# Kernel optimization log

Hardware: AMD Instinct MI355X
Metric: run time of the kernel (lower is better)

The kernel has to match this reference:

```python
import jax, jax.numpy as jnp
import numpy as np

N_NODES = 50000
N_EDGES = 800000
FEA_DIM = 128
N_LAYER = 3
ACTOR_H = 512
N_GRAPHS = 64


def gcn_conv(x, src, dst, W, b, n_nodes):
    """PyG GCNConv: add self-loops, symmetric deg normalization, linear, scatter-add.
    out[i] = sum_{j->i} d_j^{-1/2} d_i^{-1/2} (x_j W) + d_i^{-1} (x_i W) + b
    where d_i = in_degree(i) + 1 (self-loop included)."""
    h = x @ W  # [N, F]
    deg = jax.ops.segment_sum(jnp.ones(src.shape[0], x.dtype), dst, num_segments=n_nodes) + 1.0
    dinv = jax.lax.rsqrt(deg)  # [N]
    coef = (dinv[src] * dinv[dst])[:, None]  # [E, 1]
    agg = jax.ops.segment_sum(h[src] * coef, dst, num_segments=n_nodes)  # gather-scale-scatter
    agg = agg + h * (dinv * dinv)[:, None]  # self-loop term
    return agg + b


def setup_inputs() -> dict:
    key = jax.random.key(0)
    ks = jax.random.split(key, 12)
    x = jax.random.normal(ks[0], (N_NODES, FEA_DIM), dtype=jnp.float32)
    edge_index = jax.random.randint(ks[1], (2, N_EDGES), 0, N_NODES, dtype=jnp.int32)
    batch = jnp.sort(jax.random.randint(ks[2], (N_NODES,), 0, N_GRAPHS, dtype=jnp.int32))
    s = 1.0 / np.sqrt(FEA_DIM)
    conv_W = jax.random.normal(ks[3], (N_LAYER, FEA_DIM, FEA_DIM), dtype=jnp.float32) * s
    conv_b = jnp.zeros((N_LAYER, FEA_DIM), dtype=jnp.float32)
    fea_w1 = jax.random.normal(ks[4], (FEA_DIM, ACTOR_H), dtype=jnp.float32) * s
    fea_b1 = jnp.zeros((ACTOR_H,), dtype=jnp.float32)
    fea_w2 = jax.random.normal(ks[5], (ACTOR_H, FEA_DIM), dtype=jnp.float32) * (1.0 / np.sqrt(ACTOR_H))
    fea_b2 = jnp.zeros((FEA_DIM,), dtype=jnp.float32)
    node_w = jax.random.normal(ks[6], (FEA_DIM, 1), dtype=jnp.float32) * s
    node_b = jnp.zeros((1,), dtype=jnp.float32)
    return {"x": x, "edge_index": edge_index, "batch": batch,
            "conv_W": conv_W, "conv_b": conv_b,
            "fea_w1": fea_w1, "fea_b1": fea_b1,
            "fea_w2": fea_w2, "fea_b2": fea_b2,
            "node_w": node_w, "node_b": node_b}


def reference(x, edge_index, batch, conv_W, conv_b, fea_w1, fea_b1, fea_w2, fea_b2, node_w, node_b):
    src, dst = edge_index[0], edge_index[1]
    n_nodes = x.shape[0]
    for l in range(N_LAYER):  # fixed small layer loop
        x = jax.nn.relu(gcn_conv(x, src, dst, conv_W[l], conv_b[l], n_nodes))
    node_prob = jnp.squeeze(x @ node_w + node_b, axis=-1)  # [N]
    # global mean pool over graphs
    sums = jax.ops.segment_sum(x, batch, num_segments=N_GRAPHS)  # [G, F]
    cnts = jax.ops.segment_sum(jnp.ones(n_nodes, x.dtype), batch, num_segments=N_GRAPHS)
    fea = sums / jnp.maximum(cnts, 1.0)[:, None]
    fea = jax.nn.relu(fea @ fea_w1 + fea_b1)
    fea_prob = fea @ fea_w2 + fea_b2  # [G, F]
    return (node_prob, fea_prob)
```

## Files before the change

### kernel.cpp

```cpp
#include <hip/hip_runtime.h>

#define N_NODES 50000
#define N_EDGES 800000
#define FEA 128
#define NL 3
#define AH 512
#define NG 64
#define NBLK 196

typedef short bf16x8 __attribute__((ext_vector_type(8)));
typedef float f32x4 __attribute__((ext_vector_type(4)));
typedef uint  u32x4 __attribute__((ext_vector_type(4)));

__device__ __forceinline__ ushort f2bf(float f) {
    uint u = __float_as_uint(f);
    uint r = u + 0x7FFFu + ((u >> 16) & 1u);
    return (ushort)(r >> 16);
}
__device__ __forceinline__ float bf2f(ushort u) {
    return __uint_as_float((uint)u << 16);
}

#define HS ((size_t)(N_NODES + 1) * 32)
#define XS ((size_t)N_NODES * 32)

#define DA 3125
#define DB (DA + 3125)
#define DC (DB + 192)
#define DD (DC + 1)
__global__ __launch_bounds__(256) void k_deg_prep(const int* __restrict__ dst,
                                                  int* __restrict__ deg,
                                                  ushort* __restrict__ rank,
                                                  const float* __restrict__ x,
                                                  ushort* __restrict__ X,
                                                  const float* __restrict__ convW,
                                                  ushort* __restrict__ WhiT,
                                                  ushort* __restrict__ WloT,
                                                  ushort* __restrict__ H) {
    int blk = blockIdx.x;
    if (blk < DA) {
        int i = blk * 256 + threadIdx.x;
        rank[i] = (ushort)atomicAdd(&deg[dst[i]], 1);
    } else if (blk < DB) {
        int i = (blk - DA) * 256 + threadIdx.x;
        int node = i >> 4, c8 = i & 15;
        const float* xr = x + (size_t)node * FEA + c8 * 8;
        float4 u0 = *(const float4*)xr;
        float4 u1 = *(const float4*)(xr + 4);
        float xs[8] = {u0.x, u0.y, u0.z, u0.w, u1.x, u1.y, u1.z, u1.w};
        ushort hs[8];
#pragma unroll
        for (int k = 0; k < 8; ++k) hs[k] = f2bf(xs[k]);
        u32x4 hv;
        hv.x = (uint)hs[0] | ((uint)hs[1] << 16);
        hv.y = (uint)hs[2] | ((uint)hs[3] << 16);
        hv.z = (uint)hs[4] | ((uint)hs[5] << 16);
        hv.w = (uint)hs[6] | ((uint)hs[7] << 16);
        *(u32x4*)(X + (size_t)(c8 >> 2) * XS + (size_t)node * 32 + (c8 & 3) * 8) = hv;
    } else if (blk < DC) {
        int t = (blk - DB) * 256 + threadIdx.x;
        int l = t >> 14, r = t & 16383;
        int k = r >> 7, c = r & 127;
        float w = convW[t];
        ushort h = f2bf(w);
        WhiT[(size_t)l * 16384 + c * FEA + k] = h;
        WloT[(size_t)l * 16384 + c * FEA + k] = f2bf(w - bf2f(h));
    } else {
        if (threadIdx.x < 64) {
            int c = threadIdx.x >> 4, j = threadIdx.x & 15;
            ((uint*)H)[(size_t)c * (HS / 2) + (size_t)N_NODES * 16 + j] = 0;
        }
    }
}

__device__ __forceinline__ int block_scan_incl(int v, int* wsum) {
    int lane = threadIdx.x & 63, w = threadIdx.x >> 6;
    int s = v;
#pragma unroll
    for (int off = 1; off < 64; off <<= 1) {
        int t = __shfl_up(s, off);
        if (lane >= off) s += t;
    }
    if (lane == 63) wsum[w] = s;
    __syncthreads();
    int woff = 0;
    for (int k = 0; k < w; ++k) woff += wsum[k];
    return woff + s;
}

__global__ __launch_bounds__(256) void k_scan1(const int* __restrict__ deg,
                                               int* __restrict__ rowptr,
                                               int* __restrict__ bsum,
                                               float* __restrict__ dinv) {
    __shared__ int wsum[4];
    int i = blockIdx.x * 256 + threadIdx.x;
    int v = (i < N_NODES) ? deg[i] : 0;
    int pv = (v + 7) & ~7;
    int incl = block_scan_incl(pv, wsum);
    if (i < N_NODES) {
        rowptr[i] = incl - pv;
        dinv[i] = rsqrtf((float)v + 1.0f);
    }
    if (threadIdx.x == 255) bsum[blockIdx.x] = incl;
}

__global__ __launch_bounds__(256) void k_scan2(int* __restrict__ bsum,
                                               int* __restrict__ boff,
                                               int* __restrict__ rowptr) {
    __shared__ int wsum[4];
    int v = (threadIdx.x < NBLK) ? bsum[threadIdx.x] : 0;
    int incl = block_scan_incl(v, wsum);
    if (threadIdx.x < NBLK) boff[threadIdx.x] = incl - v;
    if (threadIdx.x == NBLK - 1) rowptr[N_NODES] = incl;
}

__global__ __launch_bounds__(256) void k_scan3(int* __restrict__ rowptr,
                                               const int* __restrict__ boff) {
    int i = blockIdx.x * 256 + threadIdx.x;
    if (i < N_NODES) rowptr[i] += boff[blockIdx.x];
}

#define FA 3125
#define FB (FA + NBLK)
#define FC (FB + NBLK)
__global__ __launch_bounds__(256) void k_fill2(const int* __restrict__ src,
                                               const int* __restrict__ dst,
                                               const int* __restrict__ rowptr,
                                               const ushort* __restrict__ rank,
                                               const int* __restrict__ deg,
                                               const int* __restrict__ batch,
                                               ushort* __restrict__ eidx,
                                               int* __restrict__ gstart) {
    int blk = blockIdx.x;
    if (blk < FA) {
        int e = blk * 256 + threadIdx.x;
        eidx[rowptr[dst[e]] + (int)rank[e]] = (ushort)src[e];
    } else if (blk < FB) {
        int i = (blk - FA) * 256 + threadIdx.x;
        if (i < N_NODES) {
            int d = deg[i], r = rowptr[i];
            int pd = (d + 7) & ~7;
            for (int k = d; k < pd; ++k) eidx[r + k] = (ushort)N_NODES;
        }
    } else {
        int i = (blk - FB) * 256 + threadIdx.x;
        if (i < N_NODES) {
            int b = batch[i];
            int bp = (i == 0) ? -1 : batch[i - 1];
            for (int g = bp + 1; g <= b; ++g) gstart[g] = i;
            if (i == N_NODES - 1)
                for (int g = b + 1; g <= NG; ++g) gstart[g] = N_NODES;
        }
    }
}

__global__ __launch_bounds__(256) void k_gemm(const ushort* __restrict__ X,
                                              const ushort* __restrict__ WhiT,
                                              const ushort* __restrict__ WloT,
                                              const float* __restrict__ dinv,
                                              ushort* __restrict__ H) {
    const int wv = threadIdx.x >> 6;
    const int lane = threadIdx.x & 63;
    const int lr = lane & 15;
    const int lk = lane >> 4;

    bf16x8 bhi[2][4], blo[2][4];
#pragma unroll
    for (int ct = 0; ct < 2; ++ct) {
        int col = wv * 32 + ct * 16 + lr;
#pragma unroll
        for (int kf = 0; kf < 4; ++kf) {
            bhi[ct][kf] = *(const bf16x8*)(WhiT + (size_t)col * FEA + kf * 32 + lk * 8);
            blo[ct][kf] = *(const bf16x8*)(WloT + (size_t)col * FEA + kf * 32 + lk * 8);
        }
    }

    for (int rt = blockIdx.x; rt < N_NODES / 16; rt += gridDim.x) {
        int r0 = rt * 16;
        bf16x8 a[4];
#pragma unroll
        for (int kf = 0; kf < 4; ++kf) {
            a[kf] = *(const bf16x8*)(X + (size_t)kf * XS + (size_t)(r0 + lr) * 32 + lk * 8);
        }
        f32x4 acc0 = {0.f, 0.f, 0.f, 0.f};
        f32x4 acc1 = {0.f, 0.f, 0.f, 0.f};
#pragma unroll
        for (int kf = 0; kf < 4; ++kf) {
            acc0 = __builtin_amdgcn_mfma_f32_16x16x32_bf16(a[kf], bhi[0][kf], acc0, 0, 0, 0);
            acc0 = __builtin_amdgcn_mfma_f32_16x16x32_bf16(a[kf], blo[0][kf], acc0, 0, 0, 0);
            acc1 = __builtin_amdgcn_mfma_f32_16x16x32_bf16(a[kf], bhi[1][kf], acc1, 0, 0, 0);
            acc1 = __builtin_amdgcn_mfma_f32_16x16x32_bf16(a[kf], blo[1][kf], acc1, 0, 0, 0);
        }
#pragma unroll
        for (int reg = 0; reg < 4; ++reg) {
            int orow = r0 + lk * 4 + reg;
            float s = dinv[orow];
            H[(size_t)wv * HS + (size_t)orow * 32 + lr]      = f2bf(acc0[reg] * s);
            H[(size_t)wv * HS + (size_t)orow * 32 + 16 + lr] = f2bf(acc1[reg] * s);
        }
    }
}

#define GNPB 64
#define GNB ((N_NODES + GNPB - 1) / GNPB)
__global__ __launch_bounds__(256) void k_gather(const int* __restrict__ rowptr,
                                                const ushort* __restrict__ eidx,
                                                const float* __restrict__ dinv,
                                                const ushort* __restrict__ H,
                                                const float* __restrict__ b,
                                                ushort* __restrict__ X) {
    int c = blockIdx.x & 3;
    int node = (blockIdx.x >> 2) * GNPB + (threadIdx.x >> 2);
    int l4 = threadIdx.x & 3;
    if (node >= N_NODES) return;
    const uint4* Hs = (const uint4*)H + (size_t)c * (N_NODES + 1) * 4;
    int r0 = rowptr[node], r1 = rowptr[node + 1];

    float a[8] = {0.f, 0.f, 0.f, 0.f, 0.f, 0.f, 0.f, 0.f};
#define ACC8(u)                                                              \
    do {                                                                     \
        a[0] += __uint_as_float((u).x << 16);                                \
        a[1] += __uint_as_float((u).x & 0xffff0000u);                        \
        a[2] += __uint_as_float((u).y << 16);                                \
        a[3] += __uint_as_float((u).y & 0xffff0000u);                        \
        a[4] += __uint_as_float((u).z << 16);                                \
        a[5] += __uint_as_float((u).z & 0xffff0000u);                        \
        a[6] += __uint_as_float((u).w << 16);                                \
        a[7] += __uint_as_float((u).w & 0xffff0000u);                        \
    } while (0)

    uint4 sv = Hs[(size_t)node * 4 + l4];
    ACC8(sv);

    for (int j = r0; j < r1; j += 8) {
        uint4 ev = *(const uint4*)(eidx + j);
        int s0 = ev.x & 0xffff, s1 = ev.x >> 16;
        int s2 = ev.y & 0xffff, s3 = ev.y >> 16;
        int s4 = ev.z & 0xffff, s5 = ev.z >> 16;
        int s6 = ev.w & 0xffff, s7 = ev.w >> 16;
        uint4 h0 = Hs[(size_t)s0 * 4 + l4];
        uint4 h1 = Hs[(size_t)s1 * 4 + l4];
        uint4 h2 = Hs[(size_t)s2 * 4 + l4];
        uint4 h3 = Hs[(size_t)s3 * 4 + l4];
        uint4 h4 = Hs[(size_t)s4 * 4 + l4];
        uint4 h5 = Hs[(size_t)s5 * 4 + l4];
        uint4 h6 = Hs[(size_t)s6 * 4 + l4];
        uint4 h7 = Hs[(size_t)s7 * 4 + l4];
        ACC8(h0); ACC8(h1); ACC8(h2); ACC8(h3);
        ACC8(h4); ACC8(h5); ACC8(h6); ACC8(h7);
    }
#undef ACC8

    float di = dinv[node];
    const float4* b4 = (const float4*)(b + c * 32 + l4 * 8);
    float4 bb0 = b4[0], bb1 = b4[1];
    float o[8];
    o[0] = fmaxf(a[0] * di + bb0.x, 0.f);
    o[1] = fmaxf(a[1] * di + bb0.y, 0.f);
    o[2] = fmaxf(a[2] * di + bb0.z, 0.f);
    o[3] = fmaxf(a[3] * di + bb0.w, 0.f);
    o[4] = fmaxf(a[4] * di + bb1.x, 0.f);
    o[5] = fmaxf(a[5] * di + bb1.y, 0.f);
    o[6] = fmaxf(a[6] * di + bb1.z, 0.f);
    o[7] = fmaxf(a[7] * di + bb1.w, 0.f);

    ushort hs[8];
#pragma unroll
    for (int i = 0; i < 8; ++i) hs[i] = f2bf(o[i]);
    u32x4 hv;
    hv.x = (uint)hs[0] | ((uint)hs[1] << 16);
    hv.y = (uint)hs[2] | ((uint)hs[3] << 16);
    hv.z = (uint)hs[4] | ((uint)hs[5] << 16);
    hv.w = (uint)hs[6] | ((uint)hs[7] << 16);
    __builtin_nontemporal_store(hv, (u32x4*)(X + (size_t)c * XS + (size_t)node * 32 + l4 * 8));
}

__global__ __launch_bounds__(256) void k_pool(const ushort* __restrict__ X,
                                              const int* __restrict__ gstart,
                                              const float* __restrict__ nw,
                                              const float* __restrict__ nbp,
                                              float* __restrict__ out_node,
                                              float* __restrict__ psum_part) {
    int g = blockIdx.x >> 4, p = blockIdx.x & 15;
    int s = gstart[g], e = gstart[g + 1];
    int len = e - s;
    int lp = (len + 15) >> 4;
    int ps = s + p * lp, pe = min(ps + lp, e);
    int q = threadIdx.x >> 6, lane = threadIdx.x & 63;
    const uint* hb = (const uint*)X + (size_t)(lane >> 4) * (XS / 2) + (lane & 15);
    float2 w = ((const float2*)nw)[lane];
    float nbv = nbp[0];
    float2 acc = {0.f, 0.f};
    for (int node = ps + q; node < pe; node += 4) {
        uint hv = hb[(size_t)node * 16];
        float2 v;
        v.x = bf2f((ushort)hv);
        v.y = bf2f((ushort)(hv >> 16));
        acc.x += v.x; acc.y += v.y;
        float dot = v.x * w.x + v.y * w.y;
#pragma unroll
        for (int off = 32; off; off >>= 1) dot += __shfl_down(dot, off);
        if (lane == 0) out_node[node] = dot + nbv;
    }
    __shared__ float lds[4 * FEA];
    lds[q * FEA + lane * 2 + 0] = acc.x;
    lds[q * FEA + lane * 2 + 1] = acc.y;
    __syncthreads();
    if (threadIdx.x < FEA) {
        psum_part[(size_t)blockIdx.x * FEA + threadIdx.x] =
            lds[threadIdx.x] + lds[FEA + threadIdx.x] +
            lds[2 * FEA + threadIdx.x] + lds[3 * FEA + threadIdx.x];
    }
}

__global__ __launch_bounds__(256) void k_mlp1(const float* __restrict__ psum_part,
                                              const int* __restrict__ gstart,
                                              const float* __restrict__ w1,
                                              const float* __restrict__ b1,
                                              float* __restrict__ h1ws) {
    __shared__ float feas[NG * 132];
    for (int idx = threadIdx.x; idx < NG * FEA; idx += 256) {
        int g = idx >> 7, f = idx & 127;
        const float* pp = psum_part + (size_t)g * 16 * FEA + f;
        float sum = 0.f;
#pragma unroll
        for (int p = 0; p < 16; ++p) sum += pp[p * FEA];
        float cnt = fmaxf((float)(gstart[g + 1] - gstart[g]), 1.0f);
        feas[g * 132 + f] = sum / cnt;
    }
    __syncthreads();
    int g = threadIdx.x >> 2, jj = threadIdx.x & 3;
    int j = blockIdx.x * 4 + jj;
    const float* fr = feas + g * 132;
    float a0 = 0.f, a1 = 0.f, a2 = 0.f, a3 = 0.f;
#pragma unroll 8
    for (int k = 0; k < FEA; k += 4) {
        a0 += fr[k + 0] * w1[(k + 0) * AH + j];
        a1 += fr[k + 1] * w1[(k + 1) * AH + j];
        a2 += fr[k + 2] * w1[(k + 2) * AH + j];
        a3 += fr[k + 3] * w1[(k + 3) * AH + j];
    }
    h1ws[(size_t)g * AH + j] = fmaxf((a0 + a1) + (a2 + a3) + b1[j], 0.f);
}

__global__ __launch_bounds__(256) void k_mlp2(const float* __restrict__ h1ws,
                                              const float* __restrict__ w2,
                                              const float* __restrict__ b2,
                                              float* __restrict__ out_fea) {
    int f = blockIdx.x;
    int g = threadIdx.x >> 2, q = threadIdx.x & 3;
    const float* hr = h1ws + (size_t)g * AH + q * 128;
    const float* wr = w2 + (size_t)q * 128 * FEA + f;
    float a0 = 0.f, a1 = 0.f, a2 = 0.f, a3 = 0.f;
#pragma unroll 8
    for (int k = 0; k < 128; k += 4) {
        a0 += hr[k + 0] * wr[(k + 0) * FEA];
        a1 += hr[k + 1] * wr[(k + 1) * FEA];
        a2 += hr[k + 2] * wr[(k + 2) * FEA];
        a3 += hr[k + 3] * wr[(k + 3) * FEA];
    }
    float p = (a0 + a1) + (a2 + a3);
    p += __shfl_xor(p, 1);
    p += __shfl_xor(p, 2);
    if (q == 0) out_fea[(size_t)g * FEA + f] = p + b2[f];
}

extern "C" void kernel_launch(void* const* d_in, const int* in_sizes, int n_in,
                              void* d_out, int out_size, void* d_ws, size_t ws_size,
                              hipStream_t stream) {
    const float* x     = (const float*)d_in[0];
    const int*   ei    = (const int*)d_in[1];
    const int*   batch = (const int*)d_in[2];
    const float* convW = (const float*)d_in[3];
    const float* convb = (const float*)d_in[4];
    const float* w1    = (const float*)d_in[5];
    const float* b1    = (const float*)d_in[6];
    const float* w2    = (const float*)d_in[7];
    const float* b2    = (const float*)d_in[8];
    const float* nw    = (const float*)d_in[9];
    const float* nb    = (const float*)d_in[10];
    float* out = (float*)d_out;

    char* wsb = (char*)d_ws;
    int*    deg    = (int*)wsb;
    float*  dinv   = (float*)(wsb + 50048ll * 4);
    int*    rowptr = (int*)(wsb + 100096ll * 4);
    int*    bsum   = (int*)(wsb + 150144ll * 4);
    int*    boff   = (int*)(wsb + 150344ll * 4);
    int*    gstart = (int*)(wsb + 150544ll * 4);
    int*    rankw  = (int*)(wsb + 150656ll * 4);
    ushort* rank   = (ushort*)rankw;
    float*  h1ws   = (float*)rankw;
    ushort* eidx   = (ushort*)(wsb + 950656ll * 4);
    ushort* H      = (ushort*)(wsb + 1600672ll * 4);
    ushort* X      = (ushort*)(wsb + 4800736ll * 4);
    float*  psum_part = (float*)(wsb + 11200736ll * 4);
    ushort* WhiT   = (ushort*)psum_part;
    ushort* WloT   = WhiT + 49152;

    const int* srcp = ei;
    const int* dstp = ei + N_EDGES;

    hipMemsetAsync(deg, 0, N_NODES * sizeof(int), stream);
    k_deg_prep<<<DD, 256, 0, stream>>>(dstp, deg, rank, x, X, convW, WhiT, WloT, H);
    k_scan1<<<NBLK, 256, 0, stream>>>(deg, rowptr, bsum, dinv);
    k_scan2<<<1, 256, 0, stream>>>(bsum, boff, rowptr);
    k_scan3<<<NBLK, 256, 0, stream>>>(rowptr, boff);
    k_fill2<<<FC, 256, 0, stream>>>(srcp, dstp, rowptr, rank, deg, batch, eidx, gstart);

    for (int l = 0; l < NL; ++l) {
        k_gemm<<<1024, 256, 0, stream>>>(X, WhiT + (size_t)l * 16384,
                                         WloT + (size_t)l * 16384, dinv, H);
        k_gather<<<GNB * 4, 256, 0, stream>>>(
            rowptr, eidx, dinv, H, convb + (size_t)l * FEA, X);
    }

    k_pool<<<NG * 16, 256, 0, stream>>>(X, gstart, nw, nb, out, psum_part);
    k_mlp1<<<128, 256, 0, stream>>>(psum_part, gstart, w1, b1, h1ws);
    k_mlp2<<<128, 256, 0, stream>>>(h1ws, w2, b2, out + N_NODES);
}
```

Baseline: 225.6 us.

## Sort gather nodes into degree buckets to balance wavefront work

Computes a 16-bin histogram of padded in-degree per scan block, scans it into global bucket offsets, and builds a permutation that groups nodes by degree. The gather kernel then processes nodes in permuted order, so lanes in a wavefront handle similar edge counts and spend less time idle on divergent loop lengths. In exchange, the gather pays an extra indirection through perm and loses spatial locality of node order in its X writes and H self-row reads. The scan kernels also gain shared-memory atomics and a larger histogram scan.

```diff
diff --git a/kernel.cpp b/kernel.cpp
--- a/kernel.cpp
+++ b/kernel.cpp
@@ -91,8 +91,11 @@
 __global__ __launch_bounds__(256) void k_scan1(const int* __restrict__ deg,
                                                int* __restrict__ rowptr,
                                                int* __restrict__ bsum,
-                                               float* __restrict__ dinv) {
+                                               float* __restrict__ dinv,
+                                               int* __restrict__ bhist) {
     __shared__ int wsum[4];
+    __shared__ int bh[16];
+    if (threadIdx.x < 16) bh[threadIdx.x] = 0;
     int i = blockIdx.x * 256 + threadIdx.x;
     int v = (i < N_NODES) ? deg[i] : 0;
     int pv = (v + 7) & ~7;
@@ -100,24 +103,62 @@
     if (i < N_NODES) {
         rowptr[i] = incl - pv;
         dinv[i] = rsqrtf((float)v + 1.0f);
+        int bin = min(pv >> 3, 15);
+        atomicAdd(&bh[bin], 1);
     }
     if (threadIdx.x == 255) bsum[blockIdx.x] = incl;
-}
-
+    __syncthreads();
+    if (threadIdx.x < 16) bhist[threadIdx.x * NBLK + blockIdx.x] = bh[threadIdx.x];
+}
+
+#define BH_N (16 * NBLK)
 __global__ __launch_bounds__(256) void k_scan2(int* __restrict__ bsum,
                                                int* __restrict__ boff,
-                                               int* __restrict__ rowptr) {
+                                               int* __restrict__ rowptr,
+                                               const int* __restrict__ bhist,
+                                               int* __restrict__ boffs) {
     __shared__ int wsum[4];
     int v = (threadIdx.x < NBLK) ? bsum[threadIdx.x] : 0;
     int incl = block_scan_incl(v, wsum);
     if (threadIdx.x < NBLK) boff[threadIdx.x] = incl - v;
     if (threadIdx.x == NBLK - 1) rowptr[N_NODES] = incl;
+    __syncthreads();
+    __shared__ int wsum2[4];
+    int base = threadIdx.x * 13;
+    int vals[13];
+    int mysum = 0;
+#pragma unroll
+    for (int k = 0; k < 13; ++k) {
+        int idx = base + k;
+        int t = (idx < BH_N) ? bhist[idx] : 0;
+        vals[k] = mysum;
+        mysum += t;
+    }
+    int incl2 = block_scan_incl(mysum, wsum2);
+    int excl = incl2 - mysum;
+#pragma unroll
+    for (int k = 0; k < 13; ++k) {
+        int idx = base + k;
+        if (idx < BH_N) boffs[idx] = excl + vals[k];
+    }
 }
 
 __global__ __launch_bounds__(256) void k_scan3(int* __restrict__ rowptr,
-                                               const int* __restrict__ boff) {
+                                               const int* __restrict__ boff,
+                                               const int* __restrict__ deg,
+                                               const int* __restrict__ boffs,
+                                               int* __restrict__ perm) {
+    __shared__ int cur[16];
+    if (threadIdx.x < 16) cur[threadIdx.x] = boffs[threadIdx.x * NBLK + blockIdx.x];
+    __syncthreads();
     int i = blockIdx.x * 256 + threadIdx.x;
-    if (i < N_NODES) rowptr[i] += boff[blockIdx.x];
+    if (i < N_NODES) {
+        rowptr[i] += boff[blockIdx.x];
+        int pv = (deg[i] + 7) & ~7;
+        int bin = min(pv >> 3, 15);
+        int slot = atomicAdd(&cur[bin], 1);
+        perm[slot] = i;
+    }
 }
 
 #define FA 3125
@@ -208,11 +249,13 @@
                                                 const float* __restrict__ dinv,
                                                 const ushort* __restrict__ H,
                                                 const float* __restrict__ b,
+                                                const int* __restrict__ perm,
                                                 ushort* __restrict__ X) {
     int c = blockIdx.x & 3;
-    int node = (blockIdx.x >> 2) * GNPB + (threadIdx.x >> 2);
+    int pi = (blockIdx.x >> 2) * GNPB + (threadIdx.x >> 2);
     int l4 = threadIdx.x & 3;
-    if (node >= N_NODES) return;
+    if (pi >= N_NODES) return;
+    int node = perm[pi];
     const uint4* Hs = (const uint4*)H + (size_t)c * (N_NODES + 1) * 4;
     int r0 = rowptr[node], r1 = rowptr[node + 1];
 
@@ -388,7 +431,10 @@
     int*    bsum   = (int*)(wsb + 150144ll * 4);
     int*    boff   = (int*)(wsb + 150344ll * 4);
     int*    gstart = (int*)(wsb + 150544ll * 4);
-    int*    rankw  = (int*)(wsb + 150656ll * 4);
+    int*    bhist  = (int*)(wsb + 150640ll * 4);
+    int*    boffs  = (int*)(wsb + 153792ll * 4);
+    int*    perm   = (int*)(wsb + 156944ll * 4);
+    int*    rankw  = (int*)(wsb + 207008ll * 4);
     ushort* rank   = (ushort*)rankw;
     float*  h1ws   = (float*)rankw;
     ushort* eidx   = (ushort*)(wsb + 950656ll * 4);
@@ -403,16 +449,16 @@
 
     hipMemsetAsync(deg, 0, N_NODES * sizeof(int), stream);
     k_deg_prep<<<DD, 256, 0, stream>>>(dstp, deg, rank, x, X, convW, WhiT, WloT, H);
-    k_scan1<<<NBLK, 256, 0, stream>>>(deg, rowptr, bsum, dinv);
-    k_scan2<<<1, 256, 0, stream>>>(bsum, boff, rowptr);
-    k_scan3<<<NBLK, 256, 0, stream>>>(rowptr, boff);
+    k_scan1<<<NBLK, 256, 0, stream>>>(deg, rowptr, bsum, dinv, bhist);
+    k_scan2<<<1, 256, 0, stream>>>(bsum, boff, rowptr, bhist, boffs);
+    k_scan3<<<NBLK, 256, 0, stream>>>(rowptr, boff, deg, boffs, perm);
     k_fill2<<<FC, 256, 0, stream>>>(srcp, dstp, rowptr, rank, deg, batch, eidx, gstart);
 
     for (int l = 0; l < NL; ++l) {
         k_gemm<<<1024, 256, 0, stream>>>(X, WhiT + (size_t)l * 16384,
                                          WloT + (size_t)l * 16384, dinv, H);
         k_gather<<<GNB * 4, 256, 0, stream>>>(
-            rowptr, eidx, dinv, H, convb + (size_t)l * FEA, X);
+            rowptr, eidx, dinv, H, convb + (size_t)l * FEA, perm, X);
     }
 
     k_pool<<<NG * 16, 256, 0, stream>>>(X, gstart, nw, nb, out, psum_part);
```

Result: slower. 231.9 us (+2.8%).

## Privatize degree histogram into eight copies to reduce atomic contention

Applied to the files above, without the earlier changes.

The degree-count atomics are split across eight per-block-group histogram copies, indexed by block id mod 8, so fewer atomics collide on the same address. The scan kernel then sums the eight copies into the degree and writes per-copy prefix offsets, and the CSR fill adds that offset to each edge's rank. The cost is a larger memset (eight times the histogram), extra reads and writes of the hist and off arrays, and a workspace layout shift. With uniformly random destinations, contention per node is already low, so the gain is doubtful.

```diff
diff --git a/kernel.cpp b/kernel.cpp
--- a/kernel.cpp
+++ b/kernel.cpp
@@ -29,7 +29,7 @@
 #define DC (DB + 192)
 #define DD (DC + 1)
 __global__ __launch_bounds__(256) void k_deg_prep(const int* __restrict__ dst,
-                                                  int* __restrict__ deg,
+                                                  int* __restrict__ hist,
                                                   ushort* __restrict__ rank,
                                                   const float* __restrict__ x,
                                                   ushort* __restrict__ X,
@@ -40,7 +40,7 @@
     int blk = blockIdx.x;
     if (blk < DA) {
         int i = blk * 256 + threadIdx.x;
-        rank[i] = (ushort)atomicAdd(&deg[dst[i]], 1);
+        rank[i] = (ushort)atomicAdd(&hist[(blk & 7) * N_NODES + dst[i]], 1);
     } else if (blk < DB) {
         int i = (blk - DA) * 256 + threadIdx.x;
         int node = i >> 4, c8 = i & 15;
@@ -88,18 +88,29 @@
     return woff + s;
 }
 
-__global__ __launch_bounds__(256) void k_scan1(const int* __restrict__ deg,
+__global__ __launch_bounds__(256) void k_scan1(const int* __restrict__ hist,
+                                               int* __restrict__ off,
+                                               int* __restrict__ deg,
                                                int* __restrict__ rowptr,
                                                int* __restrict__ bsum,
                                                float* __restrict__ dinv) {
     __shared__ int wsum[4];
     int i = blockIdx.x * 256 + threadIdx.x;
-    int v = (i < N_NODES) ? deg[i] : 0;
-    int pv = (v + 7) & ~7;
+    int tot = 0;
+    if (i < N_NODES) {
+#pragma unroll
+        for (int y = 0; y < 8; ++y) {
+            int t = hist[y * N_NODES + i];
+            off[y * N_NODES + i] = tot;
+            tot += t;
+        }
+    }
+    int pv = (tot + 7) & ~7;
     int incl = block_scan_incl(pv, wsum);
     if (i < N_NODES) {
         rowptr[i] = incl - pv;
-        dinv[i] = rsqrtf((float)v + 1.0f);
+        deg[i] = tot;
+        dinv[i] = rsqrtf((float)tot + 1.0f);
     }
     if (threadIdx.x == 255) bsum[blockIdx.x] = incl;
 }
@@ -127,6 +138,7 @@
                                                const int* __restrict__ dst,
                                                const int* __restrict__ rowptr,
                                                const ushort* __restrict__ rank,
+                                               const int* __restrict__ off,
                                                const int* __restrict__ deg,
                                                const int* __restrict__ batch,
                                                ushort* __restrict__ eidx,
@@ -134,7 +146,9 @@
     int blk = blockIdx.x;
     if (blk < FA) {
         int e = blk * 256 + threadIdx.x;
-        eidx[rowptr[dst[e]] + (int)rank[e]] = (ushort)src[e];
+        int d = dst[e];
+        int rg = off[(blk & 7) * N_NODES + d] + (int)rank[e];
+        eidx[rowptr[d] + rg] = (ushort)src[e];
     } else if (blk < FB) {
         int i = (blk - FA) * 256 + threadIdx.x;
         if (i < N_NODES) {
@@ -388,25 +402,27 @@
     int*    bsum   = (int*)(wsb + 150144ll * 4);
     int*    boff   = (int*)(wsb + 150344ll * 4);
     int*    gstart = (int*)(wsb + 150544ll * 4);
-    int*    rankw  = (int*)(wsb + 150656ll * 4);
+    int*    hist   = (int*)(wsb + 150656ll * 4);
+    int*    off    = (int*)(wsb + 550656ll * 4);
+    int*    rankw  = (int*)(wsb + 950656ll * 4);
     ushort* rank   = (ushort*)rankw;
     float*  h1ws   = (float*)rankw;
-    ushort* eidx   = (ushort*)(wsb + 950656ll * 4);
-    ushort* H      = (ushort*)(wsb + 1600672ll * 4);
-    ushort* X      = (ushort*)(wsb + 4800736ll * 4);
-    float*  psum_part = (float*)(wsb + 11200736ll * 4);
+    ushort* eidx   = (ushort*)(wsb + 1350656ll * 4);
+    ushort* H      = (ushort*)(wsb + 2000672ll * 4);
+    ushort* X      = (ushort*)(wsb + 5200736ll * 4);
+    float*  psum_part = (float*)(wsb + 8400736ll * 4);
     ushort* WhiT   = (ushort*)psum_part;
     ushort* WloT   = WhiT + 49152;
 
     const int* srcp = ei;
     const int* dstp = ei + N_EDGES;
 
-    hipMemsetAsync(deg, 0, N_NODES * sizeof(int), stream);
-    k_deg_prep<<<DD, 256, 0, stream>>>(dstp, deg, rank, x, X, convW, WhiT, WloT, H);
-    k_scan1<<<NBLK, 256, 0, stream>>>(deg, rowptr, bsum, dinv);
+    hipMemsetAsync(hist, 0, 8 * N_NODES * sizeof(int), stream);
+    k_deg_prep<<<DD, 256, 0, stream>>>(dstp, hist, rank, x, X, convW, WhiT, WloT, H);
+    k_scan1<<<NBLK, 256, 0, stream>>>(hist, off, deg, rowptr, bsum, dinv);
     k_scan2<<<1, 256, 0, stream>>>(bsum, boff, rowptr);
     k_scan3<<<NBLK, 256, 0, stream>>>(rowptr, boff);
-    k_fill2<<<FC, 256, 0, stream>>>(srcp, dstp, rowptr, rank, deg, batch, eidx, gstart);
+    k_fill2<<<FC, 256, 0, stream>>>(srcp, dstp, rowptr, rank, off, deg, batch, eidx, gstart);
 
     for (int l = 0; l < NL; ++l) {
         k_gemm<<<1024, 256, 0, stream>>>(X, WhiT + (size_t)l * 16384,
```

After: 224.7 us. No clear change (-0.4%).

## Fuse first-layer GEMM into degree kernel and defer dinv scaling to scan

Applied to the files above, without the earlier changes.

The layer-0 GEMM now runs inside the degree-counting kernel, reading fp32 x directly and converting to bf16 in registers. This removes the separate x-to-bf16 pass and one GEMM launch. Because dinv is not known yet at that point, the H rows are scaled by dinv afterwards by extra blocks added to the scan2 kernel. The weight hi/lo bf16 split and transpose moves from a precompute pass into each GEMM block, which now does strided fp32 weight loads, and the extra read-modify-write of H adds memory traffic and a second bf16 rounding.

```diff
diff --git a/kernel.cpp b/kernel.cpp
--- a/kernel.cpp
+++ b/kernel.cpp
@@ -24,47 +24,71 @@
 #define HS ((size_t)(N_NODES + 1) * 32)
 #define XS ((size_t)N_NODES * 32)
 
-#define DA 3125
-#define DB (DA + 3125)
-#define DC (DB + 192)
-#define DD (DC + 1)
-__global__ __launch_bounds__(256) void k_deg_prep(const int* __restrict__ dst,
-                                                  int* __restrict__ deg,
-                                                  ushort* __restrict__ rank,
-                                                  const float* __restrict__ x,
-                                                  ushort* __restrict__ X,
-                                                  const float* __restrict__ convW,
-                                                  ushort* __restrict__ WhiT,
-                                                  ushort* __restrict__ WloT,
-                                                  ushort* __restrict__ H) {
+#define MA 3125
+#define MB (MA + 1024)
+#define MC (MB + 1)
+__global__ __launch_bounds__(256) void k_mega(const int* __restrict__ dst,
+                                              int* __restrict__ deg,
+                                              ushort* __restrict__ rank,
+                                              const float* __restrict__ x,
+                                              const float* __restrict__ convW0,
+                                              ushort* __restrict__ H) {
     int blk = blockIdx.x;
-    if (blk < DA) {
+    if (blk < MA) {
         int i = blk * 256 + threadIdx.x;
         rank[i] = (ushort)atomicAdd(&deg[dst[i]], 1);
-    } else if (blk < DB) {
-        int i = (blk - DA) * 256 + threadIdx.x;
-        int node = i >> 4, c8 = i & 15;
-        const float* xr = x + (size_t)node * FEA + c8 * 8;
-        float4 u0 = *(const float4*)xr;
-        float4 u1 = *(const float4*)(xr + 4);
-        float xs[8] = {u0.x, u0.y, u0.z, u0.w, u1.x, u1.y, u1.z, u1.w};
-        ushort hs[8];
-#pragma unroll
-        for (int k = 0; k < 8; ++k) hs[k] = f2bf(xs[k]);
-        u32x4 hv;
-        hv.x = (uint)hs[0] | ((uint)hs[1] << 16);
-        hv.y = (uint)hs[2] | ((uint)hs[3] << 16);
-        hv.z = (uint)hs[4] | ((uint)hs[5] << 16);
-        hv.w = (uint)hs[6] | ((uint)hs[7] << 16);
-        *(u32x4*)(X + (size_t)(c8 >> 2) * XS + (size_t)node * 32 + (c8 & 3) * 8) = hv;
-    } else if (blk < DC) {
-        int t = (blk - DB) * 256 + threadIdx.x;
-        int l = t >> 14, r = t & 16383;
-        int k = r >> 7, c = r & 127;
-        float w = convW[t];
-        ushort h = f2bf(w);
-        WhiT[(size_t)l * 16384 + c * FEA + k] = h;
-        WloT[(size_t)l * 16384 + c * FEA + k] = f2bf(w - bf2f(h));
+    } else if (blk < MB) {
+        int bid = blk - MA;
+        const int wv = threadIdx.x >> 6;
+        const int lane = threadIdx.x & 63;
+        const int lr = lane & 15;
+        const int lk = lane >> 4;
+
+        bf16x8 bhi[2][4], blo[2][4];
+#pragma unroll
+        for (int ct = 0; ct < 2; ++ct) {
+            int col = wv * 32 + ct * 16 + lr;
+#pragma unroll
+            for (int kf = 0; kf < 4; ++kf) {
+#pragma unroll
+                for (int j = 0; j < 8; ++j) {
+                    float w = convW0[(size_t)(kf * 32 + lk * 8 + j) * FEA + col];
+                    ushort h = f2bf(w);
+                    bhi[ct][kf][j] = (short)h;
+                    blo[ct][kf][j] = (short)f2bf(w - bf2f(h));
+                }
+            }
+        }
+
+        for (int rt = bid; rt < N_NODES / 16; rt += 1024) {
+            int r0 = rt * 16;
+            const float* xrow = x + (size_t)(r0 + lr) * FEA;
+            bf16x8 a[4];
+#pragma unroll
+            for (int kf = 0; kf < 4; ++kf) {
+                float4 u0 = *(const float4*)(xrow + kf * 32 + lk * 8);
+                float4 u1 = *(const float4*)(xrow + kf * 32 + lk * 8 + 4);
+                a[kf][0] = (short)f2bf(u0.x); a[kf][1] = (short)f2bf(u0.y);
+                a[kf][2] = (short)f2bf(u0.z); a[kf][3] = (short)f2bf(u0.w);
+                a[kf][4] = (short)f2bf(u1.x); a[kf][5] = (short)f2bf(u1.y);
+                a[kf][6] = (short)f2bf(u1.z); a[kf][7] = (short)f2bf(u1.w);
+            }
+            f32x4 acc0 = {0.f, 0.f, 0.f, 0.f};
+            f32x4 acc1 = {0.f, 0.f, 0.f, 0.f};
+#pragma unroll
+            for (int kf = 0; kf < 4; ++kf) {
+                acc0 = __builtin_amdgcn_mfma_f32_16x16x32_bf16(a[kf], bhi[0][kf], acc0, 0, 0, 0);
+                acc0 = __builtin_amdgcn_mfma_f32_16x16x32_bf16(a[kf], blo[0][kf], acc0, 0, 0, 0);
+                acc1 = __builtin_amdgcn_mfma_f32_16x16x32_bf16(a[kf], bhi[1][kf], acc1, 0, 0, 0);
+                acc1 = __builtin_amdgcn_mfma_f32_16x16x32_bf16(a[kf], blo[1][kf], acc1, 0, 0, 0);
+            }
+#pragma unroll
+            for (int reg = 0; reg < 4; ++reg) {
+                int orow = r0 + lk * 4 + reg;
+                H[(size_t)wv * HS + (size_t)orow * 32 + lr]      = f2bf(acc0[reg]);
+                H[(size_t)wv * HS + (size_t)orow * 32 + 16 + lr] = f2bf(acc1[reg]);
+            }
+        }
     } else {
         if (threadIdx.x < 64) {
             int c = threadIdx.x >> 4, j = threadIdx.x & 15;
@@ -104,14 +128,34 @@
     if (threadIdx.x == 255) bsum[blockIdx.x] = incl;
 }
 
+#define HU4 (4 * (N_NODES + 1) * 4)
 __global__ __launch_bounds__(256) void k_scan2(int* __restrict__ bsum,
                                                int* __restrict__ boff,
-                                               int* __restrict__ rowptr) {
-    __shared__ int wsum[4];
-    int v = (threadIdx.x < NBLK) ? bsum[threadIdx.x] : 0;
-    int incl = block_scan_incl(v, wsum);
-    if (threadIdx.x < NBLK) boff[threadIdx.x] = incl - v;
-    if (threadIdx.x == NBLK - 1) rowptr[N_NODES] = incl;
+                                               int* __restrict__ rowptr,
+                                               const float* __restrict__ dinv,
+                                               ushort* __restrict__ H) {
+    if (blockIdx.x == 0) {
+        __shared__ int wsum[4];
+        int v = (threadIdx.x < NBLK) ? bsum[threadIdx.x] : 0;
+        int incl = block_scan_incl(v, wsum);
+        if (threadIdx.x < NBLK) boff[threadIdx.x] = incl - v;
+        if (threadIdx.x == NBLK - 1) rowptr[N_NODES] = incl;
+        return;
+    }
+    int i = (blockIdx.x - 1) * 256 + threadIdx.x;
+    if (i >= HU4) return;
+    int c = i / ((N_NODES + 1) * 4);
+    int rem = i - c * ((N_NODES + 1) * 4);
+    int row = rem >> 2;
+    if (row >= N_NODES) return;
+    float dd = dinv[row];
+    u32x4 v = ((u32x4*)H)[i];
+    uint w;
+    w = v.x; v.x = (uint)f2bf(bf2f((ushort)w) * dd) | ((uint)f2bf(bf2f((ushort)(w >> 16)) * dd) << 16);
+    w = v.y; v.y = (uint)f2bf(bf2f((ushort)w) * dd) | ((uint)f2bf(bf2f((ushort)(w >> 16)) * dd) << 16);
+    w = v.z; v.z = (uint)f2bf(bf2f((ushort)w) * dd) | ((uint)f2bf(bf2f((ushort)(w >> 16)) * dd) << 16);
+    w = v.w; v.w = (uint)f2bf(bf2f((ushort)w) * dd) | ((uint)f2bf(bf2f((ushort)(w >> 16)) * dd) << 16);
+    ((u32x4*)H)[i] = v;
 }
 
 __global__ __launch_bounds__(256) void k_scan3(int* __restrict__ rowptr,
@@ -155,8 +199,7 @@
 }
 
 __global__ __launch_bounds__(256) void k_gemm(const ushort* __restrict__ X,
-                                              const ushort* __restrict__ WhiT,
-                                              const ushort* __restrict__ WloT,
+                                              const float* __restrict__ convWl,
                                               const float* __restrict__ dinv,
                                               ushort* __restrict__ H) {
     const int wv = threadIdx.x >> 6;
@@ -170,8 +213,13 @@
         int col = wv * 32 + ct * 16 + lr;
 #pragma unroll
         for (int kf = 0; kf < 4; ++kf) {
-            bhi[ct][kf] = *(const bf16x8*)(WhiT + (size_t)col * FEA + kf * 32 + lk * 8);
-            blo[ct][kf] = *(const bf16x8*)(WloT + (size_t)col * FEA + kf * 32 + lk * 8);
+#pragma unroll
+            for (int j = 0; j < 8; ++j) {
+                float w = convWl[(size_t)(kf * 32 + lk * 8 + j) * FEA + col];
+                ushort h = f2bf(w);
+                bhi[ct][kf][j] = (short)h;
+                blo[ct][kf][j] = (short)f2bf(w - bf2f(h));
+            }
         }
     }
 
@@ -394,23 +442,21 @@
     ushort* eidx   = (ushort*)(wsb + 950656ll * 4);
     ushort* H      = (ushort*)(wsb + 1600672ll * 4);
     ushort* X      = (ushort*)(wsb + 4800736ll * 4);
-    float*  psum_part = (float*)(wsb + 11200736ll * 4);
-    ushort* WhiT   = (ushort*)psum_part;
-    ushort* WloT   = WhiT + 49152;
+    float*  psum_part = (float*)(wsb + 8000736ll * 4);
 
     const int* srcp = ei;
     const int* dstp = ei + N_EDGES;
 
     hipMemsetAsync(deg, 0, N_NODES * sizeof(int), stream);
-    k_deg_prep<<<DD, 256, 0, stream>>>(dstp, deg, rank, x, X, convW, WhiT, WloT, H);
+    k_mega<<<MC, 256, 0, stream>>>(dstp, deg, rank, x, convW, H);
     k_scan1<<<NBLK, 256, 0, stream>>>(deg, rowptr, bsum, dinv);
-    k_scan2<<<1, 256, 0, stream>>>(bsum, boff, rowptr);
+    k_scan2<<<1 + (HU4 + 255) / 256, 256, 0, stream>>>(bsum, boff, rowptr, dinv, H);
     k_scan3<<<NBLK, 256, 0, stream>>>(rowptr, boff);
     k_fill2<<<FC, 256, 0, stream>>>(srcp, dstp, rowptr, rank, deg, batch, eidx, gstart);
 
-    for (int l = 0; l < NL; ++l) {
-        k_gemm<<<1024, 256, 0, stream>>>(X, WhiT + (size_t)l * 16384,
-                                         WloT + (size_t)l * 16384, dinv, H);
+    k_gather<<<GNB * 4, 256, 0, stream>>>(rowptr, eidx, dinv, H, convb, X);
+    for (int l = 1; l < NL; ++l) {
+        k_gemm<<<1024, 256, 0, stream>>>(X, convW + (size_t)l * FEA * FEA, dinv, H);
         k_gather<<<GNB * 4, 256, 0, stream>>>(
             rowptr, eidx, dinv, H, convb + (size_t)l * FEA, X);
     }
```

Result: no change. 223.7 us (-0.8%).
